# Kernel tuning notes

Hardware: AMD Instinct MI355X
Metric: run time of the kernel (lower is better)

The kernel has to match this reference:

```python
import jax, jax.numpy as jnp
import numpy as np

C = 64
G = 4          # group_number
K = 3          # kernel_size
R = 4          # reduction_ratio -> bottleneck C//R = 16
BN_EPS = 1e-3  # keras BatchNormalization default epsilon


def setup_inputs() -> dict:
    key = jax.random.key(0)
    ks = jax.random.split(key, 8)
    B, H, W = 8, 192, 192
    cr = C // R
    x = jax.random.normal(ks[0], (B, H, W, C), dtype=jnp.float32)
    # kernel_gen: Conv2D 1x1 (C -> C//R), BN, ReLU, Conv2D 1x1 (C//R -> K*K*G)
    w1 = jax.random.normal(ks[1], (C, cr), dtype=jnp.float32) * (1.0 / np.sqrt(C))
    b1 = jnp.zeros((cr,), dtype=jnp.float32)
    gamma = 1.0 + 0.1 * jax.random.normal(ks[2], (cr,), dtype=jnp.float32)
    beta = 0.1 * jax.random.normal(ks[3], (cr,), dtype=jnp.float32)
    mean = 0.1 * jax.random.normal(ks[4], (cr,), dtype=jnp.float32)
    var = jax.random.uniform(ks[5], (cr,), dtype=jnp.float32, minval=0.5, maxval=1.5)
    w2 = jax.random.normal(ks[6], (cr, K * K * G), dtype=jnp.float32) * (1.0 / np.sqrt(cr))
    b2 = jnp.zeros((K * K * G,), dtype=jnp.float32)
    return {"x": x, "w1": w1, "b1": b1, "gamma": gamma, "beta": beta,
            "mean": mean, "var": var, "w2": w2, "b2": b2}


def reference(x, w1, b1, gamma, beta, mean, var, w2, b2):
    B, H, W, Cc = x.shape
    # --- kernel generation (stride=1 -> identity pooling) ---
    t = jnp.einsum('bhwc,cd->bhwd', x, w1) + b1                 # [B,H,W,C//R]
    t = (t - mean) * jax.lax.rsqrt(var + BN_EPS) * gamma + beta  # BN (inference)
    t = jax.nn.relu(t)
    kern = jnp.einsum('bhwd,de->bhwe', t, w2) + b2               # [B,H,W,K*K*G]
    kern = kern.reshape(B, H, W, K * K, 1, G)
    # --- unfold: tf.image.extract_patches SAME, stride 1, patch order (ki,kj,C) ---
    pad = K // 2
    xp = jnp.pad(x, ((0, 0), (pad, pad), (pad, pad), (0, 0)))
    patches = jnp.stack(
        [xp[:, i:i + H, j:j + W, :] for i in range(K) for j in range(K)],
        axis=3)                                                  # [B,H,W,K*K,C]
    unfolded = patches.reshape(B, H, W, K * K, Cc // G, G)
    # --- per-pixel multiply-reduce over patch axis ---
    out = jnp.sum(kern * unfolded, axis=3)                       # [B,H,W,C//G,G]
    return out.reshape(B, H, W, Cc)
```

## Files before the change

kernel.cpp:

```cpp
#include <hip/hip_runtime.h>


#define B_   8
#define H_   192
#define W_   192
#define CR_  16
#define TH_  8
#define TW_  16
#define TILES_X (W_/TW_)
#define TILES_PER_IMG (TILES_X*(H_/TH_))
#define NBLK (B_*TILES_PER_IMG)

constexpr float BN_EPS = 1e-3f;

__device__ __forceinline__ float4 mask4(float4 k, bool v) {
    k.x = v ? k.x : 0.f;
    k.y = v ? k.y : 0.f;
    k.z = v ? k.z : 0.f;
    k.w = v ? k.w : 0.f;
    return k;
}

__device__ __forceinline__ void fma4(float4& a, const float4 k, const float4 x) {
    a.x = fmaf(k.x, x.x, a.x);
    a.y = fmaf(k.y, x.y, a.y);
    a.z = fmaf(k.z, x.z, a.z);
    a.w = fmaf(k.w, x.w, a.w);
}

#define LROWS(S, R)                                                         \
    do {                                                                    \
        int rr_ = (R);                                                      \
        if (!INTERIOR) {                                                    \
            if ((unsigned)rr_ < (unsigned)H_) rv |= (1 << (S));             \
            else                              rv &= ~(1 << (S));            \
            rr_ = rr_ < 0 ? 0 : (rr_ >= H_ ? H_ - 1 : rr_);                 \
        }                                                                   \
        const int rb_ = rr_ * (W_ * 16);                                    \
        rg[S][0] = x4[rb_ + co[0]];                                         \
        rg[S][1] = x4[rb_ + co[1]];                                         \
        rg[S][2] = x4[rb_ + co[2]];                                         \
        rg[S][3] = x4[rb_ + co[3]];                                         \
    } while (0)

#define COMP(I)                                                             \
    do {                                                                    \
        const float4* kqA_ = &s_half[((I) * 8 + 2 * j) * 9];                \
        const float4* kqB_ = kqA_ + 9;                                      \
        float4 aA_ = make_float4(0.f, 0.f, 0.f, 0.f);                       \
        float4 aB_ = make_float4(0.f, 0.f, 0.f, 0.f);                       \
        _Pragma("unroll")                                                   \
        for (int ti_ = 0; ti_ < 3; ++ti_) {                                 \
            const int s_ = ((I) + ti_) & 3;                                 \
            _Pragma("unroll")                                               \
            for (int tj_ = 0; tj_ < 3; ++tj_) {                             \
                float4 kA_ = kqA_[ti_ * 3 + tj_];                           \
                float4 kB_ = kqB_[ti_ * 3 + tj_];                           \
                if (!INTERIOR) {                                            \
                    kA_ = mask4(kA_, (((rv >> s_) & (cm >> tj_)) & 1));     \
                    kB_ = mask4(kB_, (((rv >> s_) & (cm >> (tj_ + 1))) & 1));\
                }                                                           \
                fma4(aA_, kA_, rg[s_][tj_]);                                \
                fma4(aB_, kB_, rg[s_][tj_ + 1]);                            \
            }                                                               \
        }                                                                   \
        const int ob_ = (th0 + (I)) * (W_ * 16);                            \
        o4[ob_ + (wA << 4) + c4i] = aA_;                                    \
        o4[ob_ + (wA << 4) + 16 + c4i] = aB_;                               \
    } while (0)

#define SFENCE __builtin_amdgcn_sched_barrier(0)

template <bool INTERIOR>
__device__ __forceinline__ void phase_b(const float4* __restrict__ x4,
                                        float4* __restrict__ o4,
                                        const float4* __restrict__ s_half,
                                        int th0, int tw0w, int ln)
{
    const int j   = ln >> 4;
    const int c4i = ln & 15;
    const int wA  = tw0w + 2 * j;

    int co[4];
    int cm = 0xF;
    #pragma unroll
    for (int tj = 0; tj < 4; ++tj) {
        int wc = wA - 1 + tj;
        if (!INTERIOR) {
            if ((unsigned)wc >= (unsigned)W_) cm &= ~(1 << tj);
            wc = wc < 0 ? 0 : (wc >= W_ ? W_ - 1 : wc);
        }
        co[tj] = (wc << 4) + c4i;
    }

    float4 rg[4][4];
    int rv = 0xF;

    LROWS(0, th0 - 1);
    LROWS(1, th0 + 0);
    LROWS(2, th0 + 1);
    LROWS(3, th0 + 2);

    SFENCE;
    COMP(0); LROWS(0, th0 + 3);
    SFENCE;
    COMP(1); LROWS(1, th0 + 4);
    SFENCE;
    COMP(2); LROWS(2, th0 + 5);
    SFENCE;
    COMP(3); LROWS(3, th0 + 6);
    SFENCE;
    COMP(4); LROWS(0, th0 + 7);
    SFENCE;
    COMP(5); LROWS(1, th0 + 8);
    SFENCE;
    COMP(6);
    COMP(7);
}

#undef LROWS
#undef COMP

__global__ __launch_bounds__(128, 2)
void invol_fused(const float* __restrict__ x,
                 const float* __restrict__ w1,
                 const float* __restrict__ b1,
                 const float* __restrict__ gamma,
                 const float* __restrict__ beta,
                 const float* __restrict__ mean,
                 const float* __restrict__ var,
                 const float* __restrict__ w2,
                 const float* __restrict__ b2,
                 float* __restrict__ out)
{
    __shared__ float4 s_kern[2][64 * 9];

    const int bid = blockIdx.x;
    const int img = bid & 7;
    const int tin = bid >> 3;
    const int th0 = (tin / TILES_X) * TH_;
    const int tw0 = (tin % TILES_X) * TW_;
    const int tid = threadIdx.x;
    const int wv  = tid >> 6;
    const int ln  = tid & 63;

    const float4* x4 = reinterpret_cast<const float4*>(x) +
                       (size_t)img * (H_ * W_ * 16);
    float4* o4 = reinterpret_cast<float4*>(out) +
                 (size_t)img * (H_ * W_ * 16);

    {
        const int r = ln >> 3, c8 = ln & 7;
        const int h = th0 + r, w = tw0 + 8 * wv + c8;
        const float4* xp = reinterpret_cast<const float4*>(
            x + (((size_t)((img * H_ + h) * W_ + w)) << 6));

        float td[CR_];
        #pragma unroll
        for (int d = 0; d < CR_; ++d) td[d] = 0.f;

        #pragma unroll
        for (int c4 = 0; c4 < 16; ++c4) {
            const float4 xv = xp[c4];
            const float xs[4] = {xv.x, xv.y, xv.z, xv.w};
            #pragma unroll
            for (int k = 0; k < 4; ++k) {
                const float* wr = w1 + (c4 * 4 + k) * CR_;
                #pragma unroll
                for (int d = 0; d < CR_; ++d)
                    td[d] = fmaf(xs[k], wr[d], td[d]);
            }
        }

        #pragma unroll
        for (int d = 0; d < CR_; ++d) {
            const float a = gamma[d] * rsqrtf(var[d] + BN_EPS);
            const float c = (b1[d] - mean[d]) * a + beta[d];
            td[d] = fmaxf(fmaf(td[d], a, c), 0.f);
        }

        float ke[36];
        #pragma unroll
        for (int e = 0; e < 36; ++e) ke[e] = b2[e];
        #pragma unroll
        for (int d = 0; d < CR_; ++d) {
            const float t = td[d];
            const float* wr = w2 + d * 36;
            #pragma unroll
            for (int e = 0; e < 36; ++e)
                ke[e] = fmaf(t, wr[e], ke[e]);
        }

        float4* skq = &s_kern[wv][ln * 9];
        #pragma unroll
        for (int t9 = 0; t9 < 9; ++t9)
            skq[t9] = make_float4(ke[t9 * 4 + 0], ke[t9 * 4 + 1],
                                  ke[t9 * 4 + 2], ke[t9 * 4 + 3]);
    }


    const bool interior = (th0 > 0) && (th0 + TH_ < H_) &&
                          (tw0 > 0) && (tw0 + TW_ < W_);
    if (interior)
        phase_b<true >(x4, o4, s_kern[wv], th0, tw0 + 8 * wv, ln);
    else
        phase_b<false>(x4, o4, s_kern[wv], th0, tw0 + 8 * wv, ln);
}

extern "C" void kernel_launch(void* const* d_in, const int* in_sizes, int n_in,
                              void* d_out, int out_size, void* d_ws, size_t ws_size,
                              hipStream_t stream) {
    const float* x     = (const float*)d_in[0];
    const float* w1    = (const float*)d_in[1];
    const float* b1    = (const float*)d_in[2];
    const float* gamma = (const float*)d_in[3];
    const float* beta  = (const float*)d_in[4];
    const float* mean  = (const float*)d_in[5];
    const float* var   = (const float*)d_in[6];
    const float* w2    = (const float*)d_in[7];
    const float* b2    = (const float*)d_in[8];
    float* out = (float*)d_out;

    invol_fused<<<dim3(NBLK), dim3(128), 0, stream>>>(
        x, w1, b1, gamma, beta, mean, var, w2, b2, out);
}
```

Measured before the change: 171.0 us.

## Split per-pixel kernel generation across four lanes with shuffle reduction

Kernel generation now splits each pixel's work across four lanes, each handling a 16-channel slice of the input. The partial bottleneck sums are combined with xor shuffles, and each lane then computes 9 of the 36 kernel weights. Each lane processes four pixels in a loop. The aim is coalesced contiguous loads of x and a smaller per-lane register footprint, in exchange for redundant BN/ReLU work and the shuffle overhead. Shared-memory writes become scalar and strided at 36 floats per pixel, which may cause bank conflicts.

```diff
diff --git a/kernel.cpp b/kernel.cpp
--- a/kernel.cpp
+++ b/kernel.cpp
@@ -143,6 +143,7 @@
     const int tid = threadIdx.x;
     const int wv  = tid >> 6;
     const int ln  = tid & 63;
+    const int tw0w = tw0 + 8 * wv;
 
     const float4* x4 = reinterpret_cast<const float4*>(x) +
                        (size_t)img * (H_ * W_ * 16);
@@ -150,61 +151,77 @@
                  (size_t)img * (H_ * W_ * 16);
 
     {
-        const int r = ln >> 3, c8 = ln & 7;
-        const int h = th0 + r, w = tw0 + 8 * wv + c8;
-        const float4* xp = reinterpret_cast<const float4*>(
-            x + (((size_t)((img * H_ + h) * W_ + w)) << 6));
-
-        float td[CR_];
-        #pragma unroll
-        for (int d = 0; d < CR_; ++d) td[d] = 0.f;
-
-        #pragma unroll
-        for (int c4 = 0; c4 < 16; ++c4) {
-            const float4 xv = xp[c4];
-            const float xs[4] = {xv.x, xv.y, xv.z, xv.w};
-            #pragma unroll
-            for (int k = 0; k < 4; ++k) {
-                const float* wr = w1 + (c4 * 4 + k) * CR_;
-                #pragma unroll
-                for (int d = 0; d < CR_; ++d)
-                    td[d] = fmaf(xs[k], wr[d], td[d]);
-            }
-        }
-
+        const int q     = ln & 3;
+        const int pslot = ln >> 2;
+
+        float abn[CR_], cbn[CR_];
         #pragma unroll
         for (int d = 0; d < CR_; ++d) {
-            const float a = gamma[d] * rsqrtf(var[d] + BN_EPS);
-            const float c = (b1[d] - mean[d]) * a + beta[d];
-            td[d] = fmaxf(fmaf(td[d], a, c), 0.f);
+            abn[d] = gamma[d] * rsqrtf(var[d] + BN_EPS);
+            cbn[d] = (b1[d] - mean[d]) * abn[d] + beta[d];
         }
 
-        float ke[36];
+        float* skf = reinterpret_cast<float*>(&s_kern[wv][0]);
+
         #pragma unroll
-        for (int e = 0; e < 36; ++e) ke[e] = b2[e];
-        #pragma unroll
-        for (int d = 0; d < CR_; ++d) {
-            const float t = td[d];
-            const float* wr = w2 + d * 36;
-            #pragma unroll
-            for (int e = 0; e < 36; ++e)
-                ke[e] = fmaf(t, wr[e], ke[e]);
+        for (int t = 0; t < 4; ++t) {
+            const int px = t * 16 + pslot;
+            const int h  = th0 + (px >> 3);
+            const int w  = tw0w + (px & 7);
+            const float4* xp = reinterpret_cast<const float4*>(
+                x + (((size_t)((img * H_ + h) * W_ + w)) << 6)) + q * 4;
+
+            const float4 xv[4] = {xp[0], xp[1], xp[2], xp[3]};
+
+            float tdp[CR_];
+            #pragma unroll
+            for (int d = 0; d < CR_; ++d) tdp[d] = 0.f;
+            #pragma unroll
+            for (int i = 0; i < 4; ++i) {
+                const float xs[4] = {xv[i].x, xv[i].y, xv[i].z, xv[i].w};
+                #pragma unroll
+                for (int k = 0; k < 4; ++k) {
+                    const float* wr = w1 + ((q * 4 + i) * 4 + k) * CR_;
+                    #pragma unroll
+                    for (int d = 0; d < CR_; ++d)
+                        tdp[d] = fmaf(xs[k], wr[d], tdp[d]);
+                }
+            }
+
+            #pragma unroll
+            for (int d = 0; d < CR_; ++d) tdp[d] += __shfl_xor(tdp[d], 1);
+            #pragma unroll
+            for (int d = 0; d < CR_; ++d) tdp[d] += __shfl_xor(tdp[d], 2);
+
+            #pragma unroll
+            for (int d = 0; d < CR_; ++d)
+                tdp[d] = fmaxf(fmaf(tdp[d], abn[d], cbn[d]), 0.f);
+
+            float ke[9];
+            #pragma unroll
+            for (int e = 0; e < 9; ++e) ke[e] = b2[9 * q + e];
+            #pragma unroll
+            for (int d = 0; d < CR_; ++d) {
+                const float tv = tdp[d];
+                const float* wr = w2 + d * 36 + 9 * q;
+                #pragma unroll
+                for (int e = 0; e < 9; ++e)
+                    ke[e] = fmaf(tv, wr[e], ke[e]);
+            }
+
+            float* sk = skf + px * 36 + 9 * q;
+            #pragma unroll
+            for (int e = 0; e < 9; ++e) sk[e] = ke[e];
         }
-
-        float4* skq = &s_kern[wv][ln * 9];
-        #pragma unroll
-        for (int t9 = 0; t9 < 9; ++t9)
-            skq[t9] = make_float4(ke[t9 * 4 + 0], ke[t9 * 4 + 1],
-                                  ke[t9 * 4 + 2], ke[t9 * 4 + 3]);
     }
 
 
     const bool interior = (th0 > 0) && (th0 + TH_ < H_) &&
                           (tw0 > 0) && (tw0 + TW_ < W_);
     if (interior)
-        phase_b<true >(x4, o4, s_kern[wv], th0, tw0 + 8 * wv, ln);
+        phase_b<true >(x4, o4, &s_kern[wv][0], th0, tw0w, ln);
     else
-        phase_b<false>(x4, o4, s_kern[wv], th0, tw0 + 8 * wv, ln);
+        phase_b<false>(x4, o4, &s_kern[wv][0], th0, tw0w, ln);
 }
 
 extern "C" void kernel_launch(void* const* d_in, const int* in_sizes, int n_in,
```

New measurement: 399.6 us. +133.6%, slower.
